# Kernel optimization log

Measured on AMD Instinct MI355X. Metric: run time of the kernel, lower is better.

The kernel has to match this reference:

```python
import jax, jax.numpy as jnp
import numpy as np

N_HEADS = 16
EPS = 1e-6


def setup_inputs() -> dict:
    key = jax.random.key(0)
    ks = jax.random.split(key, 8)
    B, L, D, F = 2, 2048, 1024, 4096
    s = 0.02
    return {
        "x": jax.random.normal(ks[0], (B, L, D), jnp.float32),
        "w_q": jax.random.normal(ks[1], (D, D), jnp.float32) * s,
        "w_k": jax.random.normal(ks[2], (D, D), jnp.float32) * s,
        "w_v": jax.random.normal(ks[3], (D, D), jnp.float32) * s,
        "w_o": jax.random.normal(ks[4], (D, D), jnp.float32) * s,
        "b_o": jnp.zeros((D,), jnp.float32),
        "gamma1": jnp.ones((D,), jnp.float32),
        "beta1": jnp.zeros((D,), jnp.float32),
        "gamma2": jnp.ones((D,), jnp.float32),
        "beta2": jnp.zeros((D,), jnp.float32),
        "w1": jax.random.normal(ks[5], (D, F), jnp.float32) * s,
        "b1": jnp.zeros((F,), jnp.float32),
        "w2": jax.random.normal(ks[6], (F, D), jnp.float32) * s,
        "b2": jnp.zeros((D,), jnp.float32),
    }


def _layer_norm(x, gamma, beta):
    mean = jnp.mean(x, axis=-1, keepdims=True)
    var = jnp.mean((x - mean) ** 2, axis=-1, keepdims=True)  # biased var
    return gamma * (x - mean) / jnp.sqrt(var + EPS) + beta


def _rope(x):
    # x: [B, H, L, Dk]; half-split rotation as in source
    B, H, L, Dk = x.shape
    inv_freq = 1.0 / (10000.0 ** (jnp.arange(0, Dk, 2, dtype=jnp.float32) / Dk))
    freqs = jnp.arange(L, dtype=jnp.float32)[:, None] * inv_freq  # [L, Dk/2]
    cos, sin = jnp.cos(freqs), jnp.sin(freqs)
    x1, x2 = x[..., : Dk // 2], x[..., Dk // 2 :]
    return jnp.concatenate([x1 * cos - x2 * sin, x1 * sin + x2 * cos], axis=-1)


def reference(x, w_q, w_k, w_v, w_o, b_o, gamma1, beta1, gamma2, beta2, w1, b1, w2, b2):
    B, L, D = x.shape
    H = N_HEADS
    dk = D // H

    def split(t):  # [B,L,D] -> [B,H,L,dk]
        return t.reshape(B, L, H, dk).transpose(0, 2, 1, 3)

    q = _rope(split(x @ w_q))
    k = _rope(split(x @ w_k))
    v = split(x @ w_v)

    scores = jnp.einsum("bhqd,bhkd->bhqk", q, k) / jnp.sqrt(jnp.float32(dk))
    attn = jax.nn.softmax(scores, axis=-1)
    ctx = jnp.einsum("bhqk,bhkd->bhqd", attn, v)
    ctx = ctx.transpose(0, 2, 1, 3).reshape(B, L, D)
    attn_out = ctx @ w_o + b_o

    h = _layer_norm(x + attn_out, gamma1, beta1)
    ff = jax.nn.relu(h @ w1 + b1) @ w2 + b2
    return _layer_norm(h + ff, gamma2, beta2)
```

## Files before the change

### kernel.cpp

```cpp
#include <hip/hip_runtime.h>
#include <hip/hip_bf16.h>

typedef __bf16 bf16;
typedef __bf16 bf16x8 __attribute__((ext_vector_type(8)));
typedef __bf16 bf16x4 __attribute__((ext_vector_type(4)));
typedef __bf16 bf16x2 __attribute__((ext_vector_type(2)));
typedef float f32x4 __attribute__((ext_vector_type(4)));

#define AS1 __attribute__((address_space(1)))
#define AS3 __attribute__((address_space(3)))

static __device__ __forceinline__ void gl_lds16(const bf16* g, char* lds) {
  __builtin_amdgcn_global_load_lds((const AS1 void*)g, (AS3 void*)lds, 16, 0, 0);
}

__global__ void conv_k(const float* __restrict__ in, bf16* __restrict__ out) {
  int t = blockIdx.x * blockDim.x + threadIdx.x;
  f32x4 v = *(const f32x4*)(in + (size_t)t * 4);
  bf16x4 o;
#pragma unroll
  for (int j = 0; j < 4; ++j) o[j] = (bf16)v[j];
  *(bf16x4*)(out + (size_t)t * 4) = o;
}

__global__ void transpose_k(const float* __restrict__ in, bf16* __restrict__ out,
                            int R, int C) {
  __shared__ float t[32][33];
  int c0 = blockIdx.x * 32, r0 = blockIdx.y * 32;
  int tx = threadIdx.x, ty = threadIdx.y;
#pragma unroll
  for (int i = 0; i < 32; i += 8) t[ty + i][tx] = in[(size_t)(r0 + ty + i) * C + c0 + tx];
  __syncthreads();
#pragma unroll
  for (int i = 0; i < 32; i += 8)
    out[(size_t)(c0 + ty + i) * R + r0 + tx] = (bf16)t[tx][ty + i];
}

template <bool BIAS, bool RES, bool RELU>
__global__ __launch_bounds__(256, 2) void gemm_k(
    const bf16* __restrict__ A, const bf16* __restrict__ BT,
    const float* __restrict__ bias, const bf16* __restrict__ res,
    bf16* __restrict__ C, int M, int N, int K) {
  __shared__ alignas(16) char As[128 * 128];
  __shared__ alignas(16) char Bs[128 * 128];
  const int tid = threadIdx.x;
  const int lane = tid & 63, wid = tid >> 6;
  const int wm = wid >> 1, wn = wid & 1;
  const int row0 = blockIdx.y * 128, col0 = blockIdx.x * 128;
  const int r16 = lane & 15;
  const int kb16 = (lane >> 4) * 16;

  f32x4 acc[4][4] = {};

  for (int kt = 0; kt < K; kt += 64) {
    __syncthreads();
#pragma unroll
    for (int c = 0; c < 4; ++c) {
      int beta = wid * 4096 + c * 1024 + lane * 16;
      int mr = beta >> 7;
      int ib = beta & 127;
      int k = (ib ^ ((mr & 7) << 4)) >> 1;
      gl_lds16(A + (size_t)(row0 + mr) * K + kt + k, As + wid * 4096 + c * 1024);
      gl_lds16(BT + (size_t)(col0 + mr) * K + kt + k, Bs + wid * 4096 + c * 1024);
    }
    asm volatile("s_waitcnt vmcnt(0)" ::: "memory");
    __syncthreads();

    bf16x8 af[4][2], bfr[4][2];
#pragma unroll
    for (int i = 0; i < 4; ++i)
#pragma unroll
      for (int kk = 0; kk < 2; ++kk) {
        int mr = wm * 64 + i * 16 + r16;
        af[i][kk] = *(const bf16x8*)(As + mr * 128 + ((kk * 64 + kb16) ^ ((mr & 7) << 4)));
        int nr = wn * 64 + i * 16 + r16;
        bfr[i][kk] = *(const bf16x8*)(Bs + nr * 128 + ((kk * 64 + kb16) ^ ((nr & 7) << 4)));
      }
#pragma unroll
    for (int kk = 0; kk < 2; ++kk)
#pragma unroll
      for (int mi = 0; mi < 4; ++mi)
#pragma unroll
        for (int ni = 0; ni < 4; ++ni)
          acc[mi][ni] = __builtin_amdgcn_mfma_f32_16x16x32_bf16(
              af[mi][kk], bfr[ni][kk], acc[mi][ni], 0, 0, 0);
  }

  const int rg = (lane >> 4) * 4;
#pragma unroll
  for (int mi = 0; mi < 4; ++mi)
#pragma unroll
    for (int ni = 0; ni < 4; ++ni) {
      int gcol = col0 + wn * 64 + ni * 16 + r16;
      float bv = 0.f;
      if constexpr (BIAS) bv = bias[gcol];
#pragma unroll
      for (int r = 0; r < 4; ++r) {
        int grow = row0 + wm * 64 + mi * 16 + rg + r;
        float v = acc[mi][ni][r] + bv;
        if constexpr (RES) v += (float)res[(size_t)grow * N + gcol];
        if constexpr (RELU) v = fmaxf(v, 0.f);
        C[(size_t)grow * N + gcol] = (bf16)v;
      }
    }
}

__global__ void rope_k(bf16* __restrict__ Q, bf16* __restrict__ K) {
  int t = blockIdx.x * blockDim.x + threadIdx.x;
  int i = t & 31;
  int h = (t >> 5) & 15;
  int l = (t >> 9) & 2047;
  int bi = t >> 20;
  float inv = powf(10000.0f, -(float)i * (1.0f / 32.0f));
  float f = (float)l * inv;
  float sv, cv;
  sincosf(f, &sv, &cv);
  size_t base = ((size_t)(bi * 2048 + l)) * 1024 + h * 64 + i;
  float q1 = (float)Q[base], q2 = (float)Q[base + 32];
  Q[base] = (bf16)(q1 * cv - q2 * sv);
  Q[base + 32] = (bf16)(q1 * sv + q2 * cv);
  float k1 = (float)K[base], k2 = (float)K[base + 32];
  K[base] = (bf16)(k1 * cv - k2 * sv);
  K[base + 32] = (bf16)(k1 * sv + k2 * cv);
}

__global__ __launch_bounds__(256, 4) void attn_k(
    const bf16* __restrict__ Qg, const bf16* __restrict__ Kg,
    const bf16* __restrict__ Vg, bf16* __restrict__ ctx) {
  __shared__ alignas(16) char Ks[2][64 * 128];
  __shared__ alignas(16) char Vs[2][64 * 128];

  const int tid = threadIdx.x;
  const int lane = tid & 63, wid = tid >> 6;
  const int bh = blockIdx.y;
  const int bi = bh >> 4, hi = bh & 15;
  const int q0 = blockIdx.x * 64;
  const int c = lane & 15, g = lane >> 4;
  const int kb16 = g * 16;

  const bf16* Qb = Qg + ((size_t)(bi * 2048 + q0 + wid * 16)) * 1024 + hi * 64;
  const bf16* Kb = Kg + ((size_t)(bi * 2048)) * 1024 + hi * 64;
  const bf16* Vb = Vg + ((size_t)(bi * 2048)) * 1024 + hi * 64;

  bf16x8 qf[2];
#pragma unroll
  for (int kk = 0; kk < 2; ++kk) {
    bf16x8 t = *(const bf16x8*)(Qb + (size_t)c * 1024 + kk * 32 + g * 8);
#pragma unroll
    for (int j = 0; j < 8; ++j) t[j] = (bf16)((float)t[j] * 0.125f);
    qf[kk] = t;
  }

  float mrun = -1e30f, lrun = 0.f;
  f32x4 accO[4] = {};

#pragma unroll
  for (int c2 = 0; c2 < 2; ++c2) {
    int beta = wid * 2048 + c2 * 1024 + lane * 16;
    int kv = beta >> 7, ib = beta & 127;
    int d = (ib ^ ((kv & 7) << 4)) >> 1;
    gl_lds16(Kb + (size_t)kv * 1024 + d, &Ks[0][wid * 2048 + c2 * 1024]);
  }
  {
    bf16x8 vr[2];
#pragma unroll
    for (int c2 = 0; c2 < 2; ++c2) {
      int e = tid + 256 * c2;
      vr[c2] = *(const bf16x8*)(Vb + (size_t)(e >> 3) * 1024 + (e & 7) * 8);
    }
#pragma unroll
    for (int c2 = 0; c2 < 2; ++c2) {
      int e = tid + 256 * c2;
      int kvl = e >> 3, d0 = (e & 7) * 8;
#pragma unroll
      for (int j = 0; j < 8; ++j) {
        int d = d0 + j;
        *(bf16*)(&Vs[0][d * 128 + ((kvl * 2) ^ ((((d >> 3) ^ d) & 7) << 4))]) = vr[c2][j];
      }
    }
  }
  __syncthreads();

  for (int t = 0; t < 32; ++t) {
    const int cur = t & 1, nxt = cur ^ 1;
    bf16x8 vr2[2];
    if (t + 1 < 32) {
#pragma unroll
      for (int c2 = 0; c2 < 2; ++c2) {
        int beta = wid * 2048 + c2 * 1024 + lane * 16;
        int kv = beta >> 7, ib = beta & 127;
        int d = (ib ^ ((kv & 7) << 4)) >> 1;
        gl_lds16(Kb + (size_t)((t + 1) * 64 + kv) * 1024 + d,
                 &Ks[nxt][wid * 2048 + c2 * 1024]);
      }
#pragma unroll
      for (int c2 = 0; c2 < 2; ++c2) {
        int e = tid + 256 * c2;
        vr2[c2] = *(const bf16x8*)(Vb + (size_t)((t + 1) * 64 + (e >> 3)) * 1024 + (e & 7) * 8);
      }
    }

    f32x4 sc[4];
#pragma unroll
    for (int n = 0; n < 4; ++n) {
      sc[n] = (f32x4){0.f, 0.f, 0.f, 0.f};
#pragma unroll
      for (int kk = 0; kk < 2; ++kk) {
        int kvr = n * 16 + c;
        bf16x8 kf = *(const bf16x8*)(&Ks[cur][kvr * 128 + ((kk * 64 + kb16) ^ ((kvr & 7) << 4))]);
        sc[n] = __builtin_amdgcn_mfma_f32_16x16x32_bf16(kf, qf[kk], sc[n], 0, 0, 0);
      }
    }

    float pm = sc[0][0];
#pragma unroll
    for (int n = 0; n < 4; ++n)
#pragma unroll
      for (int r = 0; r < 4; ++r) pm = fmaxf(pm, sc[n][r]);
    pm = fmaxf(pm, __shfl_xor(pm, 16));
    pm = fmaxf(pm, __shfl_xor(pm, 32));
    float mn = fmaxf(mrun, pm);
    float alpha = __expf(mrun - mn);
    mrun = mn;
    float rs = 0.f;
#pragma unroll
    for (int n = 0; n < 4; ++n)
#pragma unroll
      for (int r = 0; r < 4; ++r) {
        float pv = __expf(sc[n][r] - mn);
        sc[n][r] = pv;
        rs += pv;
      }
    rs += __shfl_xor(rs, 16);
    rs += __shfl_xor(rs, 32);
    lrun = lrun * alpha + rs;

    int P2[4][2];
#pragma unroll
    for (int n = 0; n < 4; ++n)
#pragma unroll
      for (int w = 0; w < 2; ++w) {
        bf16x2 h;
        h[0] = (bf16)sc[n][2 * w];
        h[1] = (bf16)sc[n][2 * w + 1];
        P2[n][w] = __builtin_bit_cast(int, h);
      }

    const int sA = c + ((lane & 16) << 1);
    const int sB = sA + 16;
    const bool hb = (lane & 32) != 0;
    bf16x8 pf[2];
#pragma unroll
    for (int kk = 0; kk < 2; ++kk) {
      int n0 = 2 * kk, n1 = 2 * kk + 1;
      int a0 = __shfl(P2[n0][0], sA), a1 = __shfl(P2[n0][1], sA);
      int a2 = __shfl(P2[n0][0], sB), a3 = __shfl(P2[n0][1], sB);
      int b0 = __shfl(P2[n1][0], sA), b1 = __shfl(P2[n1][1], sA);
      int b2 = __shfl(P2[n1][0], sB), b3 = __shfl(P2[n1][1], sB);
      int4 wv;
      wv.x = hb ? b0 : a0;
      wv.y = hb ? b1 : a1;
      wv.z = hb ? b2 : a2;
      wv.w = hb ? b3 : a3;
      pf[kk] = __builtin_bit_cast(bf16x8, wv);
    }

    float alo[4];
#pragma unroll
    for (int r = 0; r < 4; ++r) alo[r] = __shfl(alpha, 4 * g + r);
#pragma unroll
    for (int n = 0; n < 4; ++n)
#pragma unroll
      for (int r = 0; r < 4; ++r) accO[n][r] *= alo[r];

#pragma unroll
    for (int n = 0; n < 4; ++n)
#pragma unroll
      for (int kk = 0; kk < 2; ++kk) {
        int d = n * 16 + c;
        bf16x8 vf = *(const bf16x8*)(&Vs[cur][d * 128 + ((kk * 64 + kb16) ^ ((((d >> 3) ^ d) & 7) << 4))]);
        accO[n] = __builtin_amdgcn_mfma_f32_16x16x32_bf16(pf[kk], vf, accO[n], 0, 0, 0);
      }

    if (t + 1 < 32) {
#pragma unroll
      for (int c2 = 0; c2 < 2; ++c2) {
        int e = tid + 256 * c2;
        int kvl = e >> 3, d0 = (e & 7) * 8;
#pragma unroll
        for (int j = 0; j < 8; ++j) {
          int d = d0 + j;
          *(bf16*)(&Vs[nxt][d * 128 + ((kvl * 2) ^ ((((d >> 3) ^ d) & 7) << 4))]) = vr2[c2][j];
        }
      }
    }
    __syncthreads();
  }

  float lo[4];
#pragma unroll
  for (int r = 0; r < 4; ++r) lo[r] = __shfl(lrun, 4 * g + r);
#pragma unroll
  for (int n = 0; n < 4; ++n)
#pragma unroll
    for (int r = 0; r < 4; ++r) {
      int qrow = q0 + wid * 16 + g * 4 + r;
      int col = hi * 64 + n * 16 + c;
      ctx[((size_t)(bi * 2048 + qrow)) * 1024 + col] = (bf16)(accO[n][r] / lo[r]);
    }
}

template <bool F32OUT>
__global__ void ln_k(const bf16* __restrict__ in, const float* __restrict__ gamma,
                     const float* __restrict__ beta, void* __restrict__ outv) {
  __shared__ float red[4][2];
  int row = blockIdx.x, tid = threadIdx.x;
  const bf16* x = in + (size_t)row * 1024;
  bf16x4 v = *(const bf16x4*)(x + tid * 4);
  float f[4], s = 0.f, ss = 0.f;
#pragma unroll
  for (int j = 0; j < 4; ++j) {
    f[j] = (float)v[j];
    s += f[j];
    ss += f[j] * f[j];
  }
#pragma unroll
  for (int mk = 1; mk < 64; mk <<= 1) {
    s += __shfl_xor(s, mk);
    ss += __shfl_xor(ss, mk);
  }
  int w = tid >> 6;
  if ((tid & 63) == 0) { red[w][0] = s; red[w][1] = ss; }
  __syncthreads();
  s = red[0][0] + red[1][0] + red[2][0] + red[3][0];
  ss = red[0][1] + red[1][1] + red[2][1] + red[3][1];
  float mean = s * (1.f / 1024.f);
  float var = ss * (1.f / 1024.f) - mean * mean;
  float rinv = rsqrtf(var + 1e-6f);
  f32x4 g = *(const f32x4*)(gamma + tid * 4);
  f32x4 be = *(const f32x4*)(beta + tid * 4);
  if constexpr (F32OUT) {
    f32x4 o;
#pragma unroll
    for (int j = 0; j < 4; ++j) o[j] = g[j] * (f[j] - mean) * rinv + be[j];
    *(f32x4*)((float*)outv + (size_t)row * 1024 + tid * 4) = o;
  } else {
    bf16x4 o;
#pragma unroll
    for (int j = 0; j < 4; ++j) o[j] = (bf16)(g[j] * (f[j] - mean) * rinv + be[j]);
    *(bf16x4*)((bf16*)outv + (size_t)row * 1024 + tid * 4) = o;
  }
}

extern "C" void kernel_launch(void* const* d_in, const int* in_sizes, int n_in,
                              void* d_out, int out_size, void* d_ws, size_t ws_size,
                              hipStream_t stream) {
  const float* x = (const float*)d_in[0];
  const float* w_q = (const float*)d_in[1];
  const float* w_k = (const float*)d_in[2];
  const float* w_v = (const float*)d_in[3];
  const float* w_o = (const float*)d_in[4];
  const float* b_o = (const float*)d_in[5];
  const float* gamma1 = (const float*)d_in[6];
  const float* beta1 = (const float*)d_in[7];
  const float* gamma2 = (const float*)d_in[8];
  const float* beta2 = (const float*)d_in[9];
  const float* w1 = (const float*)d_in[10];
  const float* b1 = (const float*)d_in[11];
  const float* w2 = (const float*)d_in[12];
  const float* b2 = (const float*)d_in[13];

  char* ws = (char*)d_ws;
  const size_t MB = (size_t)1 << 20;
  bf16* wqT = (bf16*)(ws + 0 * MB);
  bf16* wkT = (bf16*)(ws + 2 * MB);
  bf16* wvT = (bf16*)(ws + 4 * MB);
  bf16* woT = (bf16*)(ws + 6 * MB);
  bf16* w1T = (bf16*)(ws + 8 * MB);
  bf16* w2T = (bf16*)(ws + 16 * MB);
  bf16* xb = (bf16*)(ws + 24 * MB);
  bf16* Q = (bf16*)(ws + 32 * MB);
  bf16* Kq = (bf16*)(ws + 40 * MB);
  bf16* V = (bf16*)(ws + 48 * MB);
  bf16* ctx = (bf16*)(ws + 56 * MB);
  bf16* r1 = (bf16*)(ws + 48 * MB);
  bf16* hb = (bf16*)(ws + 24 * MB);
  bf16* ffh = (bf16*)(ws + 32 * MB);
  bf16* s2 = (bf16*)(ws + 0 * MB);

  conv_k<<<4096, 256, 0, stream>>>(x, xb);
  dim3 tb(32, 8);
  transpose_k<<<dim3(32, 32), tb, 0, stream>>>(w_q, wqT, 1024, 1024);
  transpose_k<<<dim3(32, 32), tb, 0, stream>>>(w_k, wkT, 1024, 1024);
  transpose_k<<<dim3(32, 32), tb, 0, stream>>>(w_v, wvT, 1024, 1024);
  transpose_k<<<dim3(32, 32), tb, 0, stream>>>(w_o, woT, 1024, 1024);
  transpose_k<<<dim3(128, 32), tb, 0, stream>>>(w1, w1T, 1024, 4096);
  transpose_k<<<dim3(32, 128), tb, 0, stream>>>(w2, w2T, 4096, 1024);

  dim3 g1(8, 32);
  gemm_k<false, false, false><<<g1, 256, 0, stream>>>(xb, wqT, nullptr, nullptr, Q, 4096, 1024, 1024);
  gemm_k<false, false, false><<<g1, 256, 0, stream>>>(xb, wkT, nullptr, nullptr, Kq, 4096, 1024, 1024);
  gemm_k<false, false, false><<<g1, 256, 0, stream>>>(xb, wvT, nullptr, nullptr, V, 4096, 1024, 1024);

  rope_k<<<8192, 256, 0, stream>>>(Q, Kq);

  attn_k<<<dim3(32, 32), 256, 0, stream>>>(Q, Kq, V, ctx);

  gemm_k<true, true, false><<<g1, 256, 0, stream>>>(ctx, woT, b_o, xb, r1, 4096, 1024, 1024);
  ln_k<false><<<4096, 256, 0, stream>>>(r1, gamma1, beta1, hb);
  gemm_k<true, false, true><<<dim3(32, 32), 256, 0, stream>>>(hb, w1T, b1, nullptr, ffh, 4096, 4096, 1024);
  gemm_k<true, true, false><<<g1, 256, 0, stream>>>(ffh, w2T, b2, hb, s2, 4096, 1024, 4096);
  ln_k<true><<<4096, 256, 0, stream>>>(s2, gamma2, beta2, d_out);
}
```

Before: 433.3 us.

## Fuse prep kernels, merge QKV GEMM, double-buffer GEMM LDS, remap tiles, set MFMA priority

The conversion and transpose kernels are merged into a single prep launch. The Q, K and V projections become one GEMM with N=3072 writing an interleaved QKV buffer, and rope and attention now read it with a 3072 stride. The GEMM gains double-buffered LDS so the next tile's global_load_lds overlaps the current tile's MFMAs, plus a 1D grid with an XCD-aware block remap. Attention wraps its MFMA sections in s_setprio. Together these aim to cut launch overhead, improve L2 locality and hide load latency, at the cost of doubled GEMM LDS use, which may reduce occupancy.

Result: faster. 377.6 us (-12.9%).

```diff
diff --git a/kernel.cpp b/kernel.cpp
--- a/kernel.cpp
+++ b/kernel.cpp
@@ -14,67 +14,104 @@
   __builtin_amdgcn_global_load_lds((const AS1 void*)g, (AS3 void*)lds, 16, 0, 0);
 }
 
-__global__ void conv_k(const float* __restrict__ in, bf16* __restrict__ out) {
-  int t = blockIdx.x * blockDim.x + threadIdx.x;
-  f32x4 v = *(const f32x4*)(in + (size_t)t * 4);
-  bf16x4 o;
-#pragma unroll
-  for (int j = 0; j < 4; ++j) o[j] = (bf16)v[j];
-  *(bf16x4*)(out + (size_t)t * 4) = o;
-}
-
-__global__ void transpose_k(const float* __restrict__ in, bf16* __restrict__ out,
-                            int R, int C) {
-  __shared__ float t[32][33];
-  int c0 = blockIdx.x * 32, r0 = blockIdx.y * 32;
-  int tx = threadIdx.x, ty = threadIdx.y;
+static __device__ __forceinline__ void transp(const float* __restrict__ in,
+                                              bf16* __restrict__ out, int R, int C,
+                                              int idx, int tid, float (*t)[33]) {
+  int nbx = C >> 5;
+  int bx = idx % nbx, by = idx / nbx;
+  int c0 = bx * 32, r0 = by * 32;
+  int tx = tid & 31, ty = tid >> 5;
 #pragma unroll
   for (int i = 0; i < 32; i += 8) t[ty + i][tx] = in[(size_t)(r0 + ty + i) * C + c0 + tx];
   __syncthreads();
 #pragma unroll
   for (int i = 0; i < 32; i += 8)
     out[(size_t)(c0 + ty + i) * R + r0 + tx] = (bf16)t[tx][ty + i];
+}
+
+__global__ void prep_k(const float* __restrict__ x, const float* __restrict__ w_q,
+                       const float* __restrict__ w_k, const float* __restrict__ w_v,
+                       const float* __restrict__ w_o, const float* __restrict__ w1,
+                       const float* __restrict__ w2, bf16* __restrict__ xb,
+                       bf16* __restrict__ wqkvT, bf16* __restrict__ woT,
+                       bf16* __restrict__ w1T, bf16* __restrict__ w2T) {
+  __shared__ float t[32][33];
+  int b = blockIdx.x, tid = threadIdx.x;
+  if (b < 4096) {
+    int i = b * 256 + tid;
+    f32x4 v = *(const f32x4*)(x + (size_t)i * 4);
+    bf16x4 o;
+#pragma unroll
+    for (int j = 0; j < 4; ++j) o[j] = (bf16)v[j];
+    *(bf16x4*)(xb + (size_t)i * 4) = o;
+  } else if (b < 5120) {
+    transp(w_q, wqkvT, 1024, 1024, b - 4096, tid, t);
+  } else if (b < 6144) {
+    transp(w_k, wqkvT + 1024 * 1024, 1024, 1024, b - 5120, tid, t);
+  } else if (b < 7168) {
+    transp(w_v, wqkvT + 2048 * 1024, 1024, 1024, b - 6144, tid, t);
+  } else if (b < 8192) {
+    transp(w_o, woT, 1024, 1024, b - 7168, tid, t);
+  } else if (b < 12288) {
+    transp(w1, w1T, 1024, 4096, b - 8192, tid, t);
+  } else {
+    transp(w2, w2T, 4096, 1024, b - 12288, tid, t);
+  }
 }
 
 template <bool BIAS, bool RES, bool RELU>
 __global__ __launch_bounds__(256, 2) void gemm_k(
     const bf16* __restrict__ A, const bf16* __restrict__ BT,
     const float* __restrict__ bias, const bf16* __restrict__ res,
-    bf16* __restrict__ C, int M, int N, int K) {
-  __shared__ alignas(16) char As[128 * 128];
-  __shared__ alignas(16) char Bs[128 * 128];
+    bf16* __restrict__ C, int M, int N, int K, int nbx) {
+  __shared__ alignas(16) char As[2][128 * 128];
+  __shared__ alignas(16) char Bs[2][128 * 128];
   const int tid = threadIdx.x;
   const int lane = tid & 63, wid = tid >> 6;
   const int wm = wid >> 1, wn = wid & 1;
-  const int row0 = blockIdx.y * 128, col0 = blockIdx.x * 128;
+  const int nwg = gridDim.x;
+  const int wg = (blockIdx.x & 7) * (nwg >> 3) + (blockIdx.x >> 3);
+  const int row0 = (wg / nbx) * 128, col0 = (wg % nbx) * 128;
   const int r16 = lane & 15;
   const int kb16 = (lane >> 4) * 16;
 
   f32x4 acc[4][4] = {};
-
-  for (int kt = 0; kt < K; kt += 64) {
-    __syncthreads();
-#pragma unroll
-    for (int c = 0; c < 4; ++c) {
-      int beta = wid * 4096 + c * 1024 + lane * 16;
-      int mr = beta >> 7;
-      int ib = beta & 127;
-      int k = (ib ^ ((mr & 7) << 4)) >> 1;
-      gl_lds16(A + (size_t)(row0 + mr) * K + kt + k, As + wid * 4096 + c * 1024);
-      gl_lds16(BT + (size_t)(col0 + mr) * K + kt + k, Bs + wid * 4096 + c * 1024);
-    }
-    asm volatile("s_waitcnt vmcnt(0)" ::: "memory");
-    __syncthreads();
-
+  const int nk = K >> 6;
+
+  int smr[4], sk[4];
+#pragma unroll
+  for (int c = 0; c < 4; ++c) {
+    int beta = wid * 4096 + c * 1024 + lane * 16;
+    smr[c] = beta >> 7;
+    sk[c] = ((beta & 127) ^ ((smr[c] & 7) << 4)) >> 1;
+  }
+
+#pragma unroll
+  for (int c = 0; c < 4; ++c) {
+    gl_lds16(A + (size_t)(row0 + smr[c]) * K + sk[c], &As[0][wid * 4096 + c * 1024]);
+    gl_lds16(BT + (size_t)(col0 + smr[c]) * K + sk[c], &Bs[0][wid * 4096 + c * 1024]);
+  }
+  __syncthreads();
+
+  for (int t = 0; t < nk; ++t) {
+    const int cur = t & 1, nxt = cur ^ 1;
+    if (t + 1 < nk) {
+      const int kt = (t + 1) << 6;
+#pragma unroll
+      for (int c = 0; c < 4; ++c) {
+        gl_lds16(A + (size_t)(row0 + smr[c]) * K + kt + sk[c], &As[nxt][wid * 4096 + c * 1024]);
+        gl_lds16(BT + (size_t)(col0 + smr[c]) * K + kt + sk[c], &Bs[nxt][wid * 4096 + c * 1024]);
+      }
+    }
     bf16x8 af[4][2], bfr[4][2];
 #pragma unroll
     for (int i = 0; i < 4; ++i)
 #pragma unroll
       for (int kk = 0; kk < 2; ++kk) {
         int mr = wm * 64 + i * 16 + r16;
-        af[i][kk] = *(const bf16x8*)(As + mr * 128 + ((kk * 64 + kb16) ^ ((mr & 7) << 4)));
+        af[i][kk] = *(const bf16x8*)(&As[cur][mr * 128 + ((kk * 64 + kb16) ^ ((mr & 7) << 4))]);
         int nr = wn * 64 + i * 16 + r16;
-        bfr[i][kk] = *(const bf16x8*)(Bs + nr * 128 + ((kk * 64 + kb16) ^ ((nr & 7) << 4)));
+        bfr[i][kk] = *(const bf16x8*)(&Bs[cur][nr * 128 + ((kk * 64 + kb16) ^ ((nr & 7) << 4))]);
       }
 #pragma unroll
     for (int kk = 0; kk < 2; ++kk)
@@ -84,6 +121,7 @@
         for (int ni = 0; ni < 4; ++ni)
           acc[mi][ni] = __builtin_amdgcn_mfma_f32_16x16x32_bf16(
               af[mi][kk], bfr[ni][kk], acc[mi][ni], 0, 0, 0);
+    __syncthreads();
   }
 
   const int rg = (lane >> 4) * 4;
@@ -105,7 +143,7 @@
     }
 }
 
-__global__ void rope_k(bf16* __restrict__ Q, bf16* __restrict__ K) {
+__global__ void rope_k(bf16* __restrict__ QKV) {
   int t = blockIdx.x * blockDim.x + threadIdx.x;
   int i = t & 31;
   int h = (t >> 5) & 15;
@@ -115,18 +153,17 @@
   float f = (float)l * inv;
   float sv, cv;
   sincosf(f, &sv, &cv);
-  size_t base = ((size_t)(bi * 2048 + l)) * 1024 + h * 64 + i;
-  float q1 = (float)Q[base], q2 = (float)Q[base + 32];
-  Q[base] = (bf16)(q1 * cv - q2 * sv);
-  Q[base + 32] = (bf16)(q1 * sv + q2 * cv);
-  float k1 = (float)K[base], k2 = (float)K[base + 32];
-  K[base] = (bf16)(k1 * cv - k2 * sv);
-  K[base + 32] = (bf16)(k1 * sv + k2 * cv);
+  size_t base = ((size_t)(bi * 2048 + l)) * 3072 + h * 64 + i;
+  float q1 = (float)QKV[base], q2 = (float)QKV[base + 32];
+  QKV[base] = (bf16)(q1 * cv - q2 * sv);
+  QKV[base + 32] = (bf16)(q1 * sv + q2 * cv);
+  float k1 = (float)QKV[base + 1024], k2 = (float)QKV[base + 1056];
+  QKV[base + 1024] = (bf16)(k1 * cv - k2 * sv);
+  QKV[base + 1056] = (bf16)(k1 * sv + k2 * cv);
 }
 
 __global__ __launch_bounds__(256, 4) void attn_k(
-    const bf16* __restrict__ Qg, const bf16* __restrict__ Kg,
-    const bf16* __restrict__ Vg, bf16* __restrict__ ctx) {
+    const bf16* __restrict__ QKV, bf16* __restrict__ ctx) {
   __shared__ alignas(16) char Ks[2][64 * 128];
   __shared__ alignas(16) char Vs[2][64 * 128];
 
@@ -137,15 +174,16 @@
   const int q0 = blockIdx.x * 64;
   const int c = lane & 15, g = lane >> 4;
   const int kb16 = g * 16;
-
-  const bf16* Qb = Qg + ((size_t)(bi * 2048 + q0 + wid * 16)) * 1024 + hi * 64;
-  const bf16* Kb = Kg + ((size_t)(bi * 2048)) * 1024 + hi * 64;
-  const bf16* Vb = Vg + ((size_t)(bi * 2048)) * 1024 + hi * 64;
+  const int LD = 3072;
+
+  const bf16* Qb = QKV + ((size_t)(bi * 2048 + q0 + wid * 16)) * LD + hi * 64;
+  const bf16* Kb = QKV + ((size_t)(bi * 2048)) * LD + 1024 + hi * 64;
+  const bf16* Vb = QKV + ((size_t)(bi * 2048)) * LD + 2048 + hi * 64;
 
   bf16x8 qf[2];
 #pragma unroll
   for (int kk = 0; kk < 2; ++kk) {
-    bf16x8 t = *(const bf16x8*)(Qb + (size_t)c * 1024 + kk * 32 + g * 8);
+    bf16x8 t = *(const bf16x8*)(Qb + (size_t)c * LD + kk * 32 + g * 8);
 #pragma unroll
     for (int j = 0; j < 8; ++j) t[j] = (bf16)((float)t[j] * 0.125f);
     qf[kk] = t;
@@ -159,14 +197,14 @@
     int beta = wid * 2048 + c2 * 1024 + lane * 16;
     int kv = beta >> 7, ib = beta & 127;
     int d = (ib ^ ((kv & 7) << 4)) >> 1;
-    gl_lds16(Kb + (size_t)kv * 1024 + d, &Ks[0][wid * 2048 + c2 * 1024]);
+    gl_lds16(Kb + (size_t)kv * LD + d, &Ks[0][wid * 2048 + c2 * 1024]);
   }
   {
     bf16x8 vr[2];
 #pragma unroll
     for (int c2 = 0; c2 < 2; ++c2) {
       int e = tid + 256 * c2;
-      vr[c2] = *(const bf16x8*)(Vb + (size_t)(e >> 3) * 1024 + (e & 7) * 8);
+      vr[c2] = *(const bf16x8*)(Vb + (size_t)(e >> 3) * LD + (e & 7) * 8);
     }
 #pragma unroll
     for (int c2 = 0; c2 < 2; ++c2) {
@@ -190,17 +228,18 @@
         int beta = wid * 2048 + c2 * 1024 + lane * 16;
         int kv = beta >> 7, ib = beta & 127;
         int d = (ib ^ ((kv & 7) << 4)) >> 1;
-        gl_lds16(Kb + (size_t)((t + 1) * 64 + kv) * 1024 + d,
+        gl_lds16(Kb + (size_t)((t + 1) * 64 + kv) * LD + d,
                  &Ks[nxt][wid * 2048 + c2 * 1024]);
       }
 #pragma unroll
       for (int c2 = 0; c2 < 2; ++c2) {
         int e = tid + 256 * c2;
-        vr2[c2] = *(const bf16x8*)(Vb + (size_t)((t + 1) * 64 + (e >> 3)) * 1024 + (e & 7) * 8);
+        vr2[c2] = *(const bf16x8*)(Vb + (size_t)((t + 1) * 64 + (e >> 3)) * LD + (e & 7) * 8);
       }
     }
 
     f32x4 sc[4];
+    __builtin_amdgcn_s_setprio(1);
 #pragma unroll
     for (int n = 0; n < 4; ++n) {
       sc[n] = (f32x4){0.f, 0.f, 0.f, 0.f};
@@ -211,6 +250,7 @@
         sc[n] = __builtin_amdgcn_mfma_f32_16x16x32_bf16(kf, qf[kk], sc[n], 0, 0, 0);
       }
     }
+    __builtin_amdgcn_s_setprio(0);
 
     float pm = sc[0][0];
 #pragma unroll
@@ -273,6 +313,7 @@
 #pragma unroll
       for (int r = 0; r < 4; ++r) accO[n][r] *= alo[r];
 
+    __builtin_amdgcn_s_setprio(1);
 #pragma unroll
     for (int n = 0; n < 4; ++n)
 #pragma unroll
@@ -281,6 +322,7 @@
         bf16x8 vf = *(const bf16x8*)(&Vs[cur][d * 128 + ((kk * 64 + kb16) ^ ((((d >> 3) ^ d) & 7) << 4))]);
         accO[n] = __builtin_amdgcn_mfma_f32_16x16x32_bf16(pf[kk], vf, accO[n], 0, 0, 0);
       }
+    __builtin_amdgcn_s_setprio(0);
 
     if (t + 1 < 32) {
 #pragma unroll
@@ -372,43 +414,34 @@
 
   char* ws = (char*)d_ws;
   const size_t MB = (size_t)1 << 20;
-  bf16* wqT = (bf16*)(ws + 0 * MB);
-  bf16* wkT = (bf16*)(ws + 2 * MB);
-  bf16* wvT = (bf16*)(ws + 4 * MB);
+  bf16* wqkvT = (bf16*)(ws + 0 * MB);
   bf16* woT = (bf16*)(ws + 6 * MB);
   bf16* w1T = (bf16*)(ws + 8 * MB);
   bf16* w2T = (bf16*)(ws + 16 * MB);
   bf16* xb = (bf16*)(ws + 24 * MB);
-  bf16* Q = (bf16*)(ws + 32 * MB);
-  bf16* Kq = (bf16*)(ws + 40 * MB);
-  bf16* V = (bf16*)(ws + 48 * MB);
+  bf16* QKV = (bf16*)(ws + 32 * MB);
   bf16* ctx = (bf16*)(ws + 56 * MB);
-  bf16* r1 = (bf16*)(ws + 48 * MB);
-  bf16* hb = (bf16*)(ws + 24 * MB);
-  bf16* ffh = (bf16*)(ws + 32 * MB);
+  bf16* r1 = (bf16*)(ws + 32 * MB);
+  bf16* hb = (bf16*)(ws + 40 * MB);
+  bf16* ffh = (bf16*)(ws + 48 * MB);
   bf16* s2 = (bf16*)(ws + 0 * MB);
 
-  conv_k<<<4096, 256, 0, stream>>>(x, xb);
-  dim3 tb(32, 8);
-  transpose_k<<<dim3(32, 32), tb, 0, stream>>>(w_q, wqT, 1024, 1024);
-  transpose_k<<<dim3(32, 32), tb, 0, stream>>>(w_k, wkT, 1024, 1024);
-  transpose_k<<<dim3(32, 32), tb, 0, stream>>>(w_v, wvT, 1024, 1024);
-  transpose_k<<<dim3(32, 32), tb, 0, stream>>>(w_o, woT, 1024, 1024);
-  transpose_k<<<dim3(128, 32), tb, 0, stream>>>(w1, w1T, 1024, 4096);
-  transpose_k<<<dim3(32, 128), tb, 0, stream>>>(w2, w2T, 4096, 1024);
-
-  dim3 g1(8, 32);
-  gemm_k<false, false, false><<<g1, 256, 0, stream>>>(xb, wqT, nullptr, nullptr, Q, 4096, 1024, 1024);
-  gemm_k<false, false, false><<<g1, 256, 0, stream>>>(xb, wkT, nullptr, nullptr, Kq, 4096, 1024, 1024);
-  gemm_k<false, false, false><<<g1, 256, 0, stream>>>(xb, wvT, nullptr, nullptr, V, 4096, 1024, 1024);
-
-  rope_k<<<8192, 256, 0, stream>>>(Q, Kq);
-
-  attn_k<<<dim3(32, 32), 256, 0, stream>>>(Q, Kq, V, ctx);
-
-  gemm_k<true, true, false><<<g1, 256, 0, stream>>>(ctx, woT, b_o, xb, r1, 4096, 1024, 1024);
+  prep_k<<<16384, 256, 0, stream>>>(x, w_q, w_k, w_v, w_o, w1, w2,
+                                    xb, wqkvT, woT, w1T, w2T);
+
+  gemm_k<false, false, false><<<768, 256, 0, stream>>>(
+      xb, wqkvT, nullptr, nullptr, QKV, 4096, 3072, 1024, 24);
+
+  rope_k<<<8192, 256, 0, stream>>>(QKV);
+
+  attn_k<<<dim3(32, 32), 256, 0, stream>>>(QKV, ctx);
+
+  gemm_k<true, true, false><<<256, 256, 0, stream>>>(
+      ctx, woT, b_o, xb, r1, 4096, 1024, 1024, 8);
   ln_k<false><<<4096, 256, 0, stream>>>(r1, gamma1, beta1, hb);
-  gemm_k<true, false, true><<<dim3(32, 32), 256, 0, stream>>>(hb, w1T, b1, nullptr, ffh, 4096, 4096, 1024);
-  gemm_k<true, true, false><<<g1, 256, 0, stream>>>(ffh, w2T, b2, hb, s2, 4096, 1024, 4096);
+  gemm_k<true, false, true><<<1024, 256, 0, stream>>>(
+      hb, w1T, b1, nullptr, ffh, 4096, 4096, 1024, 32);
+  gemm_k<true, true, false><<<256, 256, 0, stream>>>(
+      ffh, w2T, b2, hb, s2, 4096, 1024, 4096, 8);
   ln_k<true><<<4096, 256, 0, stream>>>(s2, gamma2, beta2, d_out);
 }
```
